# Kernel tuning notes

Measured on AMD Instinct MI355X. Metric: run time of the kernel, lower is better.

## Reference

```python
import jax, jax.numpy as jnp
import numpy as np

B, CIN, H, W = 16, 16, 320, 320
OUT, KS, K = 16, 3, 4
HIDDEN = int(CIN * 0.25) + 1  # 5, matches attention2d
PAD = 1


def setup_inputs() -> dict:
    key = jax.random.key(0)
    k1, k2, k3, k4 = jax.random.split(key, 4)
    x = jax.random.normal(k1, (B, CIN, H, W), dtype=jnp.float32)
    # attention2d params: fc1 (1x1 conv, no bias), fc2 (1x1 conv, bias)
    w1 = jax.random.normal(k2, (HIDDEN, CIN), dtype=jnp.float32) * (2.0 / CIN) ** 0.5
    w2 = jax.random.normal(k3, (K * OUT, HIDDEN), dtype=jnp.float32) * (2.0 / HIDDEN) ** 0.5
    b2 = jnp.zeros((K * OUT,), dtype=jnp.float32)
    # expert weight bank [out, in//groups, ks, ks, K]
    weight = jax.random.normal(k4, (OUT, CIN, KS, KS, K), dtype=jnp.float32) * (1.0 / (CIN * KS * KS)) ** 0.5
    return {"x": x, "w1": w1, "w2": w2, "b2": b2, "weight": weight}


def reference(x, w1, w2, b2, weight):
    b, cin, h, w = x.shape
    out_p, cin_g, ks, _, kk = weight.shape
    # attention2d: global avg pool -> 1x1 conv -> relu -> 1x1 conv (+bias)
    pooled = x.mean(axis=(2, 3))                       # [B, Cin]
    hid = jax.nn.relu(pooled @ w1.T)                   # [B, hidden]
    attn = hid @ w2.T + b2                             # [B, K*out]
    # softmax over K experts per output channel
    s = jax.nn.softmax(attn.reshape(b, kk, out_p), axis=1)  # [B, K, out]
    # faithful to the torch conv2d grouping trick: flat layout is (k, o),
    # then group o consumes flat channels [o*K:(o+1)*K]
    coeffs = s.reshape(b, -1).reshape(b, out_p, kk)    # [B, out, K]
    # per-sample mixed kernels
    wmix = jnp.einsum('bok,ocxyk->bocxy', coeffs, weight)  # [B, out, in//g, ks, ks]
    # per-sample grouped conv via feature_group_count = B * groups (groups=1)
    xg = x.reshape(1, b * cin, h, w)
    wg = wmix.reshape(b * out_p, cin_g, ks, ks)
    out = jax.lax.conv_general_dilated(
        xg, wg, window_strides=(1, 1), padding=((PAD, PAD), (PAD, PAD)),
        feature_group_count=b, dimension_numbers=('NCHW', 'OIHW', 'NCHW'))
    return out.reshape(b, out_p, out.shape[-2], out.shape[-1])
```

## Files before the change

### kernel.cpp

```cpp
#include <hip/hip_runtime.h>
#include <hip/hip_bf16.h>
#include <math.h>

#define BB   16
#define CIN  16
#define HH   320
#define WW   320
#define OUTC 16
#define KK   4
#define HID  5
#define HWSZ (HH * WW)

#define TW   64
#define TH   16
#define LROW 66
#define LROWS 18
#define NPIX (LROWS * LROW)
#define NTASK (2 * NPIX)
#define LDSN (2 * NPIX * 8)
#define KCH  5

#define K1_BLOCKS_PER_B 100
#define K1_GROUPS_PER_BLOCK 512

#define XT_BYTES      52428800ull
#define PART_OFF      52428800ull
#define ZPAGE_OFF     52480000ull
#define WB_OFF        52480064ull
#define WS_NEED       (WB_OFF + 81920ull)

typedef __attribute__((ext_vector_type(8))) short bf16x8_t;
typedef __attribute__((ext_vector_type(4))) float f32x4_t;

static __device__ __forceinline__ unsigned short f2bf(float f) {
    union { float f; unsigned u; } x; x.f = f;
    unsigned r = x.u + 0x7FFF + ((x.u >> 16) & 1);
    return (unsigned short)(r >> 16);
}

__global__ __launch_bounds__(256)
void dg_prep_kernel(const float* __restrict__ x,
                    unsigned short* __restrict__ xT,
                    float* __restrict__ partials) {
    const int blk = blockIdx.x;
    const int b   = blk / K1_BLOCKS_PER_B;
    const int bib = blk - b * K1_BLOCKS_PER_B;
    const int half = (bib >= 50) ? 1 : 0;
    const int gbase = (bib - half * 50) * K1_GROUPS_PER_BLOCK;
    const int tid = threadIdx.x;

    const float* xb = x + ((size_t)(b * CIN + half * 8)) * HWSZ;
    unsigned short* xTb = xT + (((size_t)(b * 2 + half)) * HWSZ) * 8;

    float sums[8];
    #pragma unroll
    for (int c = 0; c < 8; ++c) sums[c] = 0.f;

    #pragma unroll 1
    for (int it = 0; it < 2; ++it) {
        const int g = gbase + it * 256 + tid;
        const int p0 = g * 4;
        f32x4_t v[8];
        #pragma unroll
        for (int c = 0; c < 8; ++c) {
            v[c] = *(const f32x4_t*)(xb + (size_t)c * HWSZ + p0);
            sums[c] += (v[c][0] + v[c][1]) + (v[c][2] + v[c][3]);
        }
        #pragma unroll
        for (int j = 0; j < 4; ++j) {
            bf16x8_t o;
            #pragma unroll
            for (int c = 0; c < 8; ++c) o[c] = (short)f2bf(v[c][j]);
            *(bf16x8_t*)(xTb + ((size_t)(p0 + j) << 3)) = o;
        }
    }

    #pragma unroll
    for (int c = 0; c < 8; ++c) {
        float s = sums[c];
        #pragma unroll
        for (int off = 32; off > 0; off >>= 1) s += __shfl_down(s, off, 64);
        sums[c] = s;
    }
    __shared__ float red[4][8];
    if ((tid & 63) == 0) {
        #pragma unroll
        for (int c = 0; c < 8; ++c) red[tid >> 6][c] = sums[c];
    }
    __syncthreads();
    if (tid < 8) {
        float t = red[0][tid] + red[1][tid] + red[2][tid] + red[3][tid];
        partials[(size_t)blk * 8 + tid] = t;
    }
}

__global__ __launch_bounds__(64)
void dg_mix2_kernel(const float* __restrict__ partials,
                    const float* __restrict__ w1,
                    const float* __restrict__ w2,
                    const float* __restrict__ b2,
                    const float* __restrict__ weight,
                    unsigned short* __restrict__ wB,
                    float* __restrict__ zpage) {
    const int b = blockIdx.x;
    const int tid = threadIdx.x;
    __shared__ float pooledSh[16];
    __shared__ float sm[64];
    __shared__ float coeff[64];

    if (tid < 16) {
        const int half = tid >> 3;
        const float* pp = partials
            + ((size_t)(b * K1_BLOCKS_PER_B + half * 50)) * 8 + (tid & 7);
        float s = 0.f;
        #pragma unroll
        for (int i = 0; i < 50; ++i) s += pp[(size_t)i * 8];
        pooledSh[tid] = s * (1.f / (float)HWSZ);
    }
    if (b == 0 && tid < 16) zpage[tid] = 0.f;
    __syncthreads();

    float pb[CIN];
    #pragma unroll
    for (int c = 0; c < CIN; ++c) pb[c] = pooledSh[c];
    float hid[HID];
    #pragma unroll
    for (int h = 0; h < HID; ++h) {
        float a = 0.f;
        #pragma unroll
        for (int c = 0; c < CIN; ++c) a = fmaf(pb[c], w1[h * CIN + c], a);
        hid[h] = fmaxf(a, 0.f);
    }
    float a = b2[tid];
    #pragma unroll
    for (int h = 0; h < HID; ++h) a = fmaf(hid[h], w2[tid * HID + h], a);
    sm[tid] = a;
    __syncthreads();

    const int oa = tid & 15;
    float a0 = sm[oa], a1 = sm[16 + oa], a2 = sm[32 + oa], a3 = sm[48 + oa];
    float m = fmaxf(fmaxf(a0, a1), fmaxf(a2, a3));
    float denom = expf(a0 - m) + expf(a1 - m) + expf(a2 - m) + expf(a3 - m);
    coeff[tid] = expf(sm[tid] - m) / denom;
    __syncthreads();

    const int o = tid & 15;
    const int kbase = (tid >> 4) * 8;
    #pragma unroll
    for (int kc = 0; kc < KCH; ++kc) {
        unsigned short frag[8];
        #pragma unroll
        for (int j = 0; j < 8; ++j) {
            const int k = kc * 32 + kbase + j;
            float v = 0.f;
            if (k < 144) {
                const int tap = k >> 4;
                const int c = k & 15;
                const float* wp = weight + (((size_t)(o * CIN + c) * 9 + tap) << 2);
                v = coeff[o * 4 + 0] * wp[0] + coeff[o * 4 + 1] * wp[1]
                  + coeff[o * 4 + 2] * wp[2] + coeff[o * 4 + 3] * wp[3];
            }
            frag[j] = f2bf(v);
        }
        unsigned short* dst = wB + (((size_t)(b * KCH + kc) * 64) + tid) * 8;
        #pragma unroll
        for (int j = 0; j < 8; ++j) dst[j] = frag[j];
    }
}

__global__ __launch_bounds__(256, 4)
void dg_conv_bf16_kernel(const unsigned short* __restrict__ xT,
                         const unsigned short* __restrict__ wB,
                         const unsigned short* __restrict__ zpage,
                         float* __restrict__ out) {
    const int b   = blockIdx.z;
    const int by0 = blockIdx.y * TH;
    const int bx0 = blockIdx.x * TW;
    const int tid = threadIdx.x;
    const int lane = tid & 63;
    const int wave = tid >> 6;

    __shared__ __align__(16) unsigned short sx[LDSN];

    bf16x8_t Bf[KCH];
    {
        const unsigned short* wBb = wB + (size_t)b * KCH * 512;
        #pragma unroll
        for (int kc = 0; kc < KCH; ++kc)
            Bf[kc] = *(const bf16x8_t*)(wBb + kc * 512 + lane * 8);
    }

    {
        const unsigned short* xTb = xT + (size_t)b * 2 * HWSZ * 8;
        #pragma unroll 1
        for (int it = 0; it < 10; ++it) {
            int t = tid + it * 256;
            if (t >= NTASK) t -= 256;
            const int half = (t >= NPIX) ? 1 : 0;
            const int P    = t - half * NPIX;
            const int row  = P / LROW;
            const int px   = P - row * LROW;
            const int gy = by0 - 1 + row;
            const int gx = bx0 - 1 + px;
            const bool valid = ((unsigned)gy < HH) && ((unsigned)gx < WW);
            const int lin = gy * WW + gx;
            const unsigned short* src = valid
                ? xTb + (((size_t)half * HWSZ + (size_t)lin) << 3)
                : zpage;
            __builtin_amdgcn_global_load_lds(
                (const __attribute__((address_space(1))) void*)src,
                (__attribute__((address_space(3))) void*)&sx[(size_t)t * 8],
                16, 0, 0);
        }
    }

    const int m     = lane & 15;
    const int quad  = lane >> 4;
    const int chalf = quad & 1;
    int dP[KCH];
    #pragma unroll
    for (int kc = 0; kc < KCH; ++kc) {
        int t = 2 * kc + (quad >> 1);
        if (t > 8) t = 8;
        dP[kc] = (t / 3 - 1) * LROW + (t % 3 - 1);
    }
    const int hofs = chalf * NPIX;

    f32x4_t acc[16];
    #pragma unroll
    for (int i = 0; i < 16; ++i) acc[i] = (f32x4_t){0.f, 0.f, 0.f, 0.f};

    __syncthreads();

    #pragma unroll
    for (int rr = 0; rr < 4; ++rr) {
        #pragma unroll
        for (int tx = 0; tx < 4; ++tx) {
            const int P0 = (4 * wave + rr + 1) * LROW + 1 + tx * 16 + m;
            #pragma unroll
            for (int kc = 0; kc < KCH; ++kc) {
                const int S = hofs + P0 + dP[kc];
                const bf16x8_t Af = *(const bf16x8_t*)&sx[(size_t)S * 8];
                acc[rr * 4 + tx] = __builtin_amdgcn_mfma_f32_16x16x32_bf16(
                    Af, Bf[kc], acc[rr * 4 + tx], 0, 0, 0);
            }
        }
    }

    const int n = lane & 15;
    float* ob = out + ((size_t)(b * OUTC + n)) * HWSZ;
    #pragma unroll
    for (int rr = 0; rr < 4; ++rr) {
        const int gy = by0 + 4 * wave + rr;
        #pragma unroll
        for (int tx = 0; tx < 4; ++tx) {
            const int gx = bx0 + tx * 16 + quad * 4;
            *(f32x4_t*)(ob + (size_t)gy * WW + gx) = acc[rr * 4 + tx];
        }
    }
}

__global__ __launch_bounds__(1024)
void dg_pool_kernel(const float* __restrict__ x, float* __restrict__ pooled) {
    const int plane = blockIdx.x;
    const float4* p4 = (const float4*)(x + (size_t)plane * HWSZ);
    float s = 0.f;
    #pragma unroll 5
    for (int i = threadIdx.x; i < HWSZ / 4; i += 1024) {
        float4 v = p4[i];
        s += (v.x + v.y) + (v.z + v.w);
    }
    #pragma unroll
    for (int off = 32; off > 0; off >>= 1) s += __shfl_down(s, off, 64);
    __shared__ float red[16];
    if ((threadIdx.x & 63) == 0) red[threadIdx.x >> 6] = s;
    __syncthreads();
    if (threadIdx.x == 0) {
        float t = 0.f;
        #pragma unroll
        for (int i = 0; i < 16; ++i) t += red[i];
        pooled[plane] = t * (1.f / (float)HWSZ);
    }
}

__global__ __launch_bounds__(64)
void dg_mix_kernel(const float* __restrict__ pooled,
                   const float* __restrict__ w1,
                   const float* __restrict__ w2,
                   const float* __restrict__ b2,
                   const float* __restrict__ weight,
                   unsigned short* __restrict__ wB) {
    const int b = blockIdx.x;
    const int tid = threadIdx.x;
    __shared__ float sm[64];
    __shared__ float coeff[64];

    float pb[CIN];
    #pragma unroll
    for (int c = 0; c < CIN; ++c) pb[c] = pooled[b * CIN + c];
    float hid[HID];
    #pragma unroll
    for (int h = 0; h < HID; ++h) {
        float a = 0.f;
        #pragma unroll
        for (int c = 0; c < CIN; ++c) a = fmaf(pb[c], w1[h * CIN + c], a);
        hid[h] = fmaxf(a, 0.f);
    }
    float a = b2[tid];
    #pragma unroll
    for (int h = 0; h < HID; ++h) a = fmaf(hid[h], w2[tid * HID + h], a);
    sm[tid] = a;
    __syncthreads();

    const int oa = tid & 15;
    float a0 = sm[oa], a1 = sm[16 + oa], a2 = sm[32 + oa], a3 = sm[48 + oa];
    float m = fmaxf(fmaxf(a0, a1), fmaxf(a2, a3));
    float denom = expf(a0 - m) + expf(a1 - m) + expf(a2 - m) + expf(a3 - m);
    coeff[tid] = expf(sm[tid] - m) / denom;
    __syncthreads();

    const int o = tid & 15;
    const int kbase = (tid >> 4) * 8;
    #pragma unroll
    for (int kc = 0; kc < KCH; ++kc) {
        unsigned short frag[8];
        #pragma unroll
        for (int j = 0; j < 8; ++j) {
            const int k = kc * 32 + kbase + j;
            float v = 0.f;
            if (k < 144) {
                const int tap = k >> 4;
                const int c = k & 15;
                const float* wp = weight + (((size_t)(o * CIN + c) * 9 + tap) << 2);
                v = coeff[o * 4 + 0] * wp[0] + coeff[o * 4 + 1] * wp[1]
                  + coeff[o * 4 + 2] * wp[2] + coeff[o * 4 + 3] * wp[3];
            }
            frag[j] = f2bf(v);
        }
        unsigned short* dst = wB + (((size_t)(b * KCH + kc) * 64) + tid) * 8;
        #pragma unroll
        for (int j = 0; j < 8; ++j) dst[j] = frag[j];
    }
}

__global__ __launch_bounds__(256, 4)
void dg_conv_kernel(const float* __restrict__ x,
                    const unsigned short* __restrict__ wB,
                    float* __restrict__ out) {
    const int b   = blockIdx.z;
    const int by0 = blockIdx.y * TH;
    const int bx0 = blockIdx.x * TW;
    const int tid = threadIdx.x;
    const int lane = tid & 63;
    const int wave = tid >> 6;

    __shared__ __align__(16) unsigned short sx[LDSN];

    bf16x8_t Bf[KCH];
    {
        const unsigned short* wBb = wB + (size_t)b * KCH * 512;
        #pragma unroll
        for (int kc = 0; kc < KCH; ++kc)
            Bf[kc] = *(const bf16x8_t*)(wBb + kc * 512 + lane * 8);
    }

    {
        const float* xb = x + (size_t)b * CIN * HWSZ;
        #pragma unroll 1
        for (int it = 0; it < 10; ++it) {
            const int t = tid + it * 256;
            if (t < NTASK) {
                const int half = (t >= NPIX) ? 1 : 0;
                const int P    = t - half * NPIX;
                const int row  = P / LROW;
                const int px   = P - row * LROW;
                const int gy = by0 - 1 + row;
                const int gx = bx0 - 1 + px;
                const bool valid = ((unsigned)gy < HH) && ((unsigned)gx < WW);
                const int gyc = valid ? gy : 0;
                const int gxc = valid ? gx : 0;
                const float* bp = xb + (size_t)(half * 8) * HWSZ
                                     + (size_t)gyc * WW + gxc;
                bf16x8_t v8;
                #pragma unroll
                for (int j = 0; j < 8; ++j) {
                    float v = valid ? bp[(size_t)j * HWSZ] : 0.f;
                    v8[j] = (short)f2bf(v);
                }
                *(bf16x8_t*)&sx[(size_t)t * 8] = v8;
            }
        }
    }

    const int m     = lane & 15;
    const int quad  = lane >> 4;
    const int chalf = quad & 1;
    int dP[KCH];
    #pragma unroll
    for (int kc = 0; kc < KCH; ++kc) {
        int t = 2 * kc + (quad >> 1);
        if (t > 8) t = 8;
        dP[kc] = (t / 3 - 1) * LROW + (t % 3 - 1);
    }
    const int hofs = chalf * NPIX;

    f32x4_t acc[16];
    #pragma unroll
    for (int i = 0; i < 16; ++i) acc[i] = (f32x4_t){0.f, 0.f, 0.f, 0.f};

    __syncthreads();

    #pragma unroll
    for (int rr = 0; rr < 4; ++rr) {
        #pragma unroll
        for (int tx = 0; tx < 4; ++tx) {
            const int P0 = (4 * wave + rr + 1) * LROW + 1 + tx * 16 + m;
            #pragma unroll
            for (int kc = 0; kc < KCH; ++kc) {
                const int S = hofs + P0 + dP[kc];
                const bf16x8_t Af = *(const bf16x8_t*)&sx[(size_t)S * 8];
                acc[rr * 4 + tx] = __builtin_amdgcn_mfma_f32_16x16x32_bf16(
                    Af, Bf[kc], acc[rr * 4 + tx], 0, 0, 0);
            }
        }
    }

    const int n = lane & 15;
    float* ob = out + ((size_t)(b * OUTC + n)) * HWSZ;
    #pragma unroll
    for (int rr = 0; rr < 4; ++rr) {
        const int gy = by0 + 4 * wave + rr;
        #pragma unroll
        for (int tx = 0; tx < 4; ++tx) {
            const int gx = bx0 + tx * 16 + quad * 4;
            *(f32x4_t*)(ob + (size_t)gy * WW + gx) = acc[rr * 4 + tx];
        }
    }
}

extern "C" void kernel_launch(void* const* d_in, const int* in_sizes, int n_in,
                              void* d_out, int out_size, void* d_ws, size_t ws_size,
                              hipStream_t stream) {
    const float* x      = (const float*)d_in[0];
    const float* w1     = (const float*)d_in[1];
    const float* w2     = (const float*)d_in[2];
    const float* b2     = (const float*)d_in[3];
    const float* weight = (const float*)d_in[4];
    float* out = (float*)d_out;

    if (ws_size >= WS_NEED) {
        unsigned short* xT       = (unsigned short*)d_ws;
        float*          partials = (float*)((char*)d_ws + PART_OFF);
        float*          zpage    = (float*)((char*)d_ws + ZPAGE_OFF);
        unsigned short* wBf      = (unsigned short*)((char*)d_ws + WB_OFF);

        dg_prep_kernel<<<BB * K1_BLOCKS_PER_B, 256, 0, stream>>>(x, xT, partials);
        dg_mix2_kernel<<<BB, 64, 0, stream>>>(partials, w1, w2, b2, weight, wBf, zpage);
        dg_conv_bf16_kernel<<<dim3(WW / TW, HH / TH, BB), 256, 0, stream>>>(
            xT, wBf, (const unsigned short*)zpage, out);
    } else {
        float* pooled = (float*)d_ws;
        unsigned short* wBf = (unsigned short*)((float*)d_ws + 256);

        dg_pool_kernel<<<BB * CIN, 1024, 0, stream>>>(x, pooled);
        dg_mix_kernel<<<BB, 64, 0, stream>>>(pooled, w1, w2, b2, weight, wBf);
        dg_conv_kernel<<<dim3(WW / TW, HH / TH, BB), 256, 0, stream>>>(x, wBf, out);
    }
}
```

Baseline: 228.7 us.

## Fuse attention and weight-mixing into conv kernel, pool via atomics

Removes the separate mix kernel. Each conv block now recomputes the attention MLP, softmax and bf16 mixed weights per wave from the pooled sums, using wave shuffles, and overlaps this with the async LDS tile load. The prep kernel accumulates channel sums with atomicAdd into a buffer zeroed by a memset, replacing the partials array and its reduction. In exchange, every block repeats the small attention and mixing work plus about 144 scattered vector weight loads, and float atomics make the pooled sums order-nondeterministic.

New measurement: 267.3 us. 16.9% more time.

```diff
diff --git a/kernel.cpp b/kernel.cpp
--- a/kernel.cpp
+++ b/kernel.cpp
@@ -24,10 +24,9 @@
 #define K1_GROUPS_PER_BLOCK 512
 
 #define XT_BYTES      52428800ull
-#define PART_OFF      52428800ull
-#define ZPAGE_OFF     52480000ull
-#define WB_OFF        52480064ull
-#define WS_NEED       (WB_OFF + 81920ull)
+#define POOLED_OFF    52428800ull
+#define ZPAGE_OFF     52429824ull
+#define WS_NEED       52430848ull
 
 typedef __attribute__((ext_vector_type(8))) short bf16x8_t;
 typedef __attribute__((ext_vector_type(4))) float f32x4_t;
@@ -41,7 +40,7 @@
 __global__ __launch_bounds__(256)
 void dg_prep_kernel(const float* __restrict__ x,
                     unsigned short* __restrict__ xT,
-                    float* __restrict__ partials) {
+                    float* __restrict__ pooled) {
     const int blk = blockIdx.x;
     const int b   = blk / K1_BLOCKS_PER_B;
     const int bib = blk - b * K1_BLOCKS_PER_B;
@@ -56,7 +55,7 @@
     #pragma unroll
     for (int c = 0; c < 8; ++c) sums[c] = 0.f;
 
-    #pragma unroll 1
+    #pragma unroll
     for (int it = 0; it < 2; ++it) {
         const int g = gbase + it * 256 + tid;
         const int p0 = g * 4;
@@ -90,89 +89,19 @@
     __syncthreads();
     if (tid < 8) {
         float t = red[0][tid] + red[1][tid] + red[2][tid] + red[3][tid];
-        partials[(size_t)blk * 8 + tid] = t;
-    }
-}
-
-__global__ __launch_bounds__(64)
-void dg_mix2_kernel(const float* __restrict__ partials,
-                    const float* __restrict__ w1,
-                    const float* __restrict__ w2,
-                    const float* __restrict__ b2,
-                    const float* __restrict__ weight,
-                    unsigned short* __restrict__ wB,
-                    float* __restrict__ zpage) {
-    const int b = blockIdx.x;
-    const int tid = threadIdx.x;
-    __shared__ float pooledSh[16];
-    __shared__ float sm[64];
-    __shared__ float coeff[64];
-
-    if (tid < 16) {
-        const int half = tid >> 3;
-        const float* pp = partials
-            + ((size_t)(b * K1_BLOCKS_PER_B + half * 50)) * 8 + (tid & 7);
-        float s = 0.f;
-        #pragma unroll
-        for (int i = 0; i < 50; ++i) s += pp[(size_t)i * 8];
-        pooledSh[tid] = s * (1.f / (float)HWSZ);
-    }
-    if (b == 0 && tid < 16) zpage[tid] = 0.f;
-    __syncthreads();
-
-    float pb[CIN];
-    #pragma unroll
-    for (int c = 0; c < CIN; ++c) pb[c] = pooledSh[c];
-    float hid[HID];
-    #pragma unroll
-    for (int h = 0; h < HID; ++h) {
-        float a = 0.f;
-        #pragma unroll
-        for (int c = 0; c < CIN; ++c) a = fmaf(pb[c], w1[h * CIN + c], a);
-        hid[h] = fmaxf(a, 0.f);
-    }
-    float a = b2[tid];
-    #pragma unroll
-    for (int h = 0; h < HID; ++h) a = fmaf(hid[h], w2[tid * HID + h], a);
-    sm[tid] = a;
-    __syncthreads();
-
-    const int oa = tid & 15;
-    float a0 = sm[oa], a1 = sm[16 + oa], a2 = sm[32 + oa], a3 = sm[48 + oa];
-    float m = fmaxf(fmaxf(a0, a1), fmaxf(a2, a3));
-    float denom = expf(a0 - m) + expf(a1 - m) + expf(a2 - m) + expf(a3 - m);
-    coeff[tid] = expf(sm[tid] - m) / denom;
-    __syncthreads();
-
-    const int o = tid & 15;
-    const int kbase = (tid >> 4) * 8;
-    #pragma unroll
-    for (int kc = 0; kc < KCH; ++kc) {
-        unsigned short frag[8];
-        #pragma unroll
-        for (int j = 0; j < 8; ++j) {
-            const int k = kc * 32 + kbase + j;
-            float v = 0.f;
-            if (k < 144) {
-                const int tap = k >> 4;
-                const int c = k & 15;
-                const float* wp = weight + (((size_t)(o * CIN + c) * 9 + tap) << 2);
-                v = coeff[o * 4 + 0] * wp[0] + coeff[o * 4 + 1] * wp[1]
-                  + coeff[o * 4 + 2] * wp[2] + coeff[o * 4 + 3] * wp[3];
-            }
-            frag[j] = f2bf(v);
-        }
-        unsigned short* dst = wB + (((size_t)(b * KCH + kc) * 64) + tid) * 8;
-        #pragma unroll
-        for (int j = 0; j < 8; ++j) dst[j] = frag[j];
+        atomicAdd(&pooled[b * CIN + half * 8 + tid], t);
     }
 }
 
 __global__ __launch_bounds__(256, 4)
-void dg_conv_bf16_kernel(const unsigned short* __restrict__ xT,
-                         const unsigned short* __restrict__ wB,
-                         const unsigned short* __restrict__ zpage,
-                         float* __restrict__ out) {
+void dg_conv_fused_kernel(const unsigned short* __restrict__ xT,
+                          const float* __restrict__ pooled,
+                          const float* __restrict__ w1,
+                          const float* __restrict__ w2,
+                          const float* __restrict__ b2,
+                          const float* __restrict__ weight,
+                          const unsigned short* __restrict__ zpage,
+                          float* __restrict__ out) {
     const int b   = blockIdx.z;
     const int by0 = blockIdx.y * TH;
     const int bx0 = blockIdx.x * TW;
@@ -181,14 +110,6 @@
     const int wave = tid >> 6;
 
     __shared__ __align__(16) unsigned short sx[LDSN];
-
-    bf16x8_t Bf[KCH];
-    {
-        const unsigned short* wBb = wB + (size_t)b * KCH * 512;
-        #pragma unroll
-        for (int kc = 0; kc < KCH; ++kc)
-            Bf[kc] = *(const bf16x8_t*)(wBb + kc * 512 + lane * 8);
-    }
 
     {
         const unsigned short* xTb = xT + (size_t)b * 2 * HWSZ * 8;
@@ -211,6 +132,57 @@
                 (const __attribute__((address_space(1))) void*)src,
                 (__attribute__((address_space(3))) void*)&sx[(size_t)t * 8],
                 16, 0, 0);
+        }
+    }
+
+    bf16x8_t Bf[KCH];
+    {
+        const float inv = 1.f / (float)HWSZ;
+        float pb[CIN];
+        #pragma unroll
+        for (int c = 0; c < CIN; ++c) pb[c] = pooled[b * CIN + c] * inv;
+        float hid[HID];
+        #pragma unroll
+        for (int h = 0; h < HID; ++h) {
+            float a = 0.f;
+            #pragma unroll
+            for (int c = 0; c < CIN; ++c) a = fmaf(pb[c], w1[h * CIN + c], a);
+            hid[h] = fmaxf(a, 0.f);
+        }
+        float a = b2[lane];
+        #pragma unroll
+        for (int h = 0; h < HID; ++h) a = fmaf(hid[h], w2[lane * HID + h], a);
+
+        const int o = lane & 15;
+        const float a0 = __shfl(a, o,      64);
+        const float a1 = __shfl(a, o + 16, 64);
+        const float a2 = __shfl(a, o + 32, 64);
+        const float a3 = __shfl(a, o + 48, 64);
+        const float m = fmaxf(fmaxf(a0, a1), fmaxf(a2, a3));
+        const float denom = expf(a0 - m) + expf(a1 - m)
+                          + expf(a2 - m) + expf(a3 - m);
+        const float coeff = expf(a - m) / denom;
+        const float c0 = __shfl(coeff, o * 4 + 0, 64);
+        const float c1 = __shfl(coeff, o * 4 + 1, 64);
+        const float c2 = __shfl(coeff, o * 4 + 2, 64);
+        const float c3 = __shfl(coeff, o * 4 + 3, 64);
+
+        const int kbase = (lane >> 4) * 8;
+        #pragma unroll
+        for (int kc = 0; kc < KCH; ++kc) {
+            #pragma unroll
+            for (int j = 0; j < 8; ++j) {
+                const int k = kc * 32 + kbase + j;
+                float v = 0.f;
+                if (k < 144) {
+                    const int tap = k >> 4;
+                    const int c = k & 15;
+                    const f32x4_t wv = *(const f32x4_t*)(
+                        weight + (((size_t)(o * CIN + c) * 9 + tap) << 2));
+                    v = c0 * wv[0] + c1 * wv[1] + c2 * wv[2] + c3 * wv[3];
+                }
+                Bf[kc][j] = (short)f2bf(v);
+            }
         }
     }
 
@@ -449,15 +421,14 @@
     float* out = (float*)d_out;
 
     if (ws_size >= WS_NEED) {
-        unsigned short* xT       = (unsigned short*)d_ws;
-        float*          partials = (float*)((char*)d_ws + PART_OFF);
-        float*          zpage    = (float*)((char*)d_ws + ZPAGE_OFF);
-        unsigned short* wBf      = (unsigned short*)((char*)d_ws + WB_OFF);
-
-        dg_prep_kernel<<<BB * K1_BLOCKS_PER_B, 256, 0, stream>>>(x, xT, partials);
-        dg_mix2_kernel<<<BB, 64, 0, stream>>>(partials, w1, w2, b2, weight, wBf, zpage);
-        dg_conv_bf16_kernel<<<dim3(WW / TW, HH / TH, BB), 256, 0, stream>>>(
-            xT, wBf, (const unsigned short*)zpage, out);
+        unsigned short* xT     = (unsigned short*)d_ws;
+        float*          pooled = (float*)((char*)d_ws + POOLED_OFF);
+        float*          zpage  = (float*)((char*)d_ws + ZPAGE_OFF);
+
+        hipMemsetAsync((char*)d_ws + POOLED_OFF, 0, 1088, stream);
+        dg_prep_kernel<<<BB * K1_BLOCKS_PER_B, 256, 0, stream>>>(x, xT, pooled);
+        dg_conv_fused_kernel<<<dim3(WW / TW, HH / TH, BB), 256, 0, stream>>>(
+            xT, pooled, w1, w2, b2, weight, (const unsigned short*)zpage, out);
     } else {
         float* pooled = (float*)d_ws;
         unsigned short* wBf = (unsigned short*)((float*)d_ws + 256);
```
